# Kernel tuning notes

Measured on AMD Instinct MI355X. Metric: run time of the kernel, lower is better.

Reference implementation:

```python
import jax, jax.numpy as jnp
import numpy as np

EPS = 1e-05

def setup_inputs() -> dict:
    key = jax.random.key(0)
    k1, k2, k3 = jax.random.split(key, 3)
    B, S, D_IN, D_OUT = 4, 2048, 4096, 12288
    x = jax.random.normal(k1, (B, S, D_IN), dtype=jnp.float32)
    weight = jax.random.normal(k2, (D_OUT, D_IN), dtype=jnp.float32) * (1.0 / np.sqrt(D_IN))
    bias = jnp.zeros((D_OUT,), dtype=jnp.float32)
    ln_weight = jnp.ones((D_IN,), dtype=jnp.float32)
    ln_bias = jnp.zeros((D_IN,), dtype=jnp.float32)
    return {"x": x, "weight": weight, "bias": bias, "ln_weight": ln_weight, "ln_bias": ln_bias}

def reference(x, weight, bias, ln_weight, ln_bias):
    # LayerNorm over last dim
    mean = jnp.mean(x, axis=-1, keepdims=True)
    var = jnp.mean(jnp.square(x - mean), axis=-1, keepdims=True)
    normed = (x - mean) * jax.lax.rsqrt(var + EPS) * ln_weight + ln_bias
    # Linear: y = normed @ W^T + b
    return jnp.einsum('bsd,od->bso', normed, weight) + bias
```

## Files before the change

kernel.cpp:

```cpp
#include <hip/hip_runtime.h>
#include <hip/hip_bf16.h>
#include <stdint.h>

typedef __attribute__((ext_vector_type(8))) short short8_t;
typedef __attribute__((ext_vector_type(4))) float f32x4;

__device__ __forceinline__ unsigned short f2bf(float f) {
  union { float f; unsigned int u; } a;
  a.f = f;
  unsigned int u = a.u;
  u += 0x7fffu + ((u >> 16) & 1u);
  return (unsigned short)(u >> 16);
}

__device__ __forceinline__ void gload_lds16(const void* g, void* l) {
  __builtin_amdgcn_global_load_lds(
      (const __attribute__((address_space(1))) void*)g,
      (__attribute__((address_space(3))) void*)l, 16, 0, 0);
}

constexpr int D_IN = 4096;

__global__ __launch_bounds__(256) void ln_bf16_kernel(
    const float* __restrict__ x, const float* __restrict__ lnw,
    const float* __restrict__ lnb, unsigned short* __restrict__ out) {
  const int row = blockIdx.x;
  const int tid = threadIdx.x;
  const float* xr = x + (size_t)row * D_IN;

  f32x4 v[4];
  float sum = 0.f, sq = 0.f;
#pragma unroll
  for (int i = 0; i < 4; ++i) {
    v[i] = __builtin_nontemporal_load(
        reinterpret_cast<const f32x4*>(xr + i * 1024 + tid * 4));
    sum += v[i][0] + v[i][1] + v[i][2] + v[i][3];
    sq += v[i][0]*v[i][0] + v[i][1]*v[i][1] + v[i][2]*v[i][2] + v[i][3]*v[i][3];
  }
#pragma unroll
  for (int off = 32; off > 0; off >>= 1) {
    sum += __shfl_down(sum, off, 64);
    sq  += __shfl_down(sq, off, 64);
  }
  __shared__ float s_sum[4], s_sq[4];
  if ((tid & 63) == 0) { s_sum[tid >> 6] = sum; s_sq[tid >> 6] = sq; }
  __syncthreads();
  const float fs = s_sum[0] + s_sum[1] + s_sum[2] + s_sum[3];
  const float fq = s_sq[0] + s_sq[1] + s_sq[2] + s_sq[3];
  const float mean = fs * (1.f / D_IN);
  const float var = fq * (1.f / D_IN) - mean * mean;
  const float rstd = rsqrtf(var + 1e-5f);

  unsigned short* orow = out + (size_t)row * D_IN;
#pragma unroll
  for (int i = 0; i < 4; ++i) {
    const int col = i * 1024 + tid * 4;
    const f32x4 w = *reinterpret_cast<const f32x4*>(lnw + col);
    const f32x4 b = *reinterpret_cast<const f32x4*>(lnb + col);
    ushort4 o;
    o.x = f2bf((v[i][0] - mean) * rstd * w[0] + b[0]);
    o.y = f2bf((v[i][1] - mean) * rstd * w[1] + b[1]);
    o.z = f2bf((v[i][2] - mean) * rstd * w[2] + b[2]);
    o.w = f2bf((v[i][3] - mean) * rstd * w[3] + b[3]);
    *reinterpret_cast<ushort4*>(orow + col) = o;
  }
}

__global__ __launch_bounds__(256) void f32_to_bf16_kernel(
    const float* __restrict__ in, unsigned short* __restrict__ out) {
  const size_t i = ((size_t)blockIdx.x * 256 + threadIdx.x) * 8;
  const f32x4 a = __builtin_nontemporal_load(reinterpret_cast<const f32x4*>(in + i));
  const f32x4 b = __builtin_nontemporal_load(reinterpret_cast<const f32x4*>(in + i + 4));
  ushort4 lo, hi;
  lo.x = f2bf(a[0]); lo.y = f2bf(a[1]); lo.z = f2bf(a[2]); lo.w = f2bf(a[3]);
  hi.x = f2bf(b[0]); hi.y = f2bf(b[1]); hi.z = f2bf(b[2]); hi.w = f2bf(b[3]);
  *reinterpret_cast<ushort4*>(out + i) = lo;
  *reinterpret_cast<ushort4*>(out + i + 4) = hi;
}


#define RDA(S, KK, ROW) \
  (*reinterpret_cast<const short8_t*>(((KK) ? aB1 : aB0) + (S)*32768 + (ROW)*128))
#define RDB(S, KK, ROW) \
  (*reinterpret_cast<const short8_t*>(((KK) ? bB1 : bB0) + (S)*32768 + (ROW)*128))

#define READ_A(S, MH)                                          \
  _Pragma("unroll") for (int m_ = 0; m_ < 4; ++m_) {           \
    af[m_][0] = RDA(S, 0, (MH)*64 + m_*16);                    \
    af[m_][1] = RDA(S, 1, (MH)*64 + m_*16);                    \
  }

#define READ_B(S, NH)                                          \
  _Pragma("unroll") for (int n_ = 0; n_ < 2; ++n_) {           \
    bfr[(NH)*2+n_][0] = RDB(S, 0, ((NH)*2+n_)*16);             \
    bfr[(NH)*2+n_][1] = RDB(S, 1, ((NH)*2+n_)*16);             \
  }

#define MFMA_Q(MH, NH)                                                         \
  _Pragma("unroll") for (int kk_ = 0; kk_ < 2; ++kk_) {                        \
    _Pragma("unroll") for (int m_ = 0; m_ < 4; ++m_) {                         \
      _Pragma("unroll") for (int n_ = 0; n_ < 2; ++n_)                         \
        acc[(MH)*4+m_][(NH)*2+n_] = __builtin_amdgcn_mfma_f32_16x16x32_bf16(   \
            af[m_][kk_], bfr[(NH)*2+n_][kk_], acc[(MH)*4+m_][(NH)*2+n_], 0, 0, 0); \
    }                                                                          \
  }

#define STAGE_A(S, U, KT) \
  gload_lds16(aSrc + (size_t)((U)*64) * K + (size_t)(KT)*64, ldsAw + (S)*32768 + (U)*8192)
#define STAGE_B(S, U, KT) \
  gload_lds16(bSrc + (size_t)((U)*64) * K + (size_t)(KT)*64, ldsBw + (S)*32768 + (U)*8192)
#define STAGE_ALL(S, KT)                                       \
  STAGE_A(S,0,KT); STAGE_A(S,1,KT); STAGE_A(S,2,KT); STAGE_A(S,3,KT); \
  STAGE_B(S,0,KT); STAGE_B(S,1,KT); STAGE_B(S,2,KT); STAGE_B(S,3,KT);

#define XREG(S)                                                \
  READ_A(S, 0) READ_B(S, 0)                                    \
  __builtin_amdgcn_s_setprio(1);                               \
  MFMA_Q(0,0)                                                  \
  READ_B(S, 1)                                                 \
  MFMA_Q(0,1)                                                  \
  READ_A(S, 1)                                                 \
  __builtin_amdgcn_s_setprio(0);                               \
  asm volatile("s_waitcnt lgkmcnt(0)" ::: "memory");           \
  __builtin_amdgcn_s_barrier();                                \
  asm volatile("" ::: "memory");

#define YREG(S, KT)                                            \
  STAGE_ALL(S, KT)                                             \
  __builtin_amdgcn_s_setprio(1);                               \
  MFMA_Q(1,0)                                                  \
  MFMA_Q(1,1)                                                  \
  __builtin_amdgcn_s_setprio(0);                               \
  asm volatile("s_waitcnt vmcnt(8)" ::: "memory");             \
  __builtin_amdgcn_s_barrier();                                \
  asm volatile("" ::: "memory");

__global__ __launch_bounds__(512, 2) void gemm_xy(
    const unsigned short* __restrict__ A,
    const unsigned short* __restrict__ B,
    const float* __restrict__ bias,
    float* __restrict__ C,
    int M, int N, int K, int NYB, int BXP) {
  extern __shared__ char smem[];
  const int tid = threadIdx.x;
  const int lane = tid & 63;
  const int wid = tid >> 6;
  const int wr = wid >> 2, wc = wid & 3;
  const int fr = lane & 15;
  const int q16 = (lane >> 4) * 16;
  const int wr128 = wr * 128;
  const int wc64 = wc * 64;

  const int id = blockIdx.x;
  const int xcd = id & 7;
  const int s = id >> 3;
  const int gsz = 8 * BXP;
  const int g = s / gsz;
  const int j = s - g * gsz;
  const int by = g * 8 + (j & 7);
  const int bx = xcd * BXP + (j >> 3);
  const int m0 = by * 256, n0 = bx * 256;

  const int s_log = (tid * 16) ^ (((tid >> 3) & 7) << 4);
  const int rsw = s_log >> 7;
  const int csw = (s_log & 127) >> 1;
  const unsigned short* aSrc = A + (size_t)(m0 + rsw) * K + csw;
  const unsigned short* bSrc = B + (size_t)(n0 + rsw) * K + csw;

  char* const ldsAw = smem + wid * 1024;
  char* const ldsBw = smem + 65536 + wid * 1024;

  const int s7 = (fr & 7) << 4;
  const char* const aB0 = smem + (wr128 + fr) * 128 + (q16 ^ s7);
  const char* const aB1 = smem + (wr128 + fr) * 128 + ((64 + q16) ^ s7);
  const char* const bB0 = smem + 65536 + (wc64 + fr) * 128 + (q16 ^ s7);
  const char* const bB1 = smem + 65536 + (wc64 + fr) * 128 + ((64 + q16) ^ s7);

  f32x4 acc[8][4] = {};
  short8_t af[4][2], bfr[4][2];

  STAGE_ALL(0, 0)
  STAGE_ALL(1, 1)
  asm volatile("s_waitcnt vmcnt(8)" ::: "memory");
  __builtin_amdgcn_s_barrier();
  asm volatile("" ::: "memory");

  const int NK = K >> 6;
  for (int t = 0; t < (NK - 2) >> 1; ++t) {
    const int k2 = 2*t + 2, k3 = 2*t + 3;
    XREG(0) YREG(0, k2)
    XREG(1) YREG(1, k3)
  }
  {
    READ_A(0, 0) READ_B(0, 0)
    __builtin_amdgcn_s_setprio(1);
    MFMA_Q(0,0)
    READ_B(0, 1)
    MFMA_Q(0,1)
    READ_A(0, 1)
    MFMA_Q(1,0)
    MFMA_Q(1,1)
    __builtin_amdgcn_s_setprio(0);
    asm volatile("s_waitcnt lgkmcnt(0)\n\ts_waitcnt vmcnt(0)" ::: "memory");
    __builtin_amdgcn_s_barrier();
    asm volatile("" ::: "memory");
    READ_A(1, 0) READ_B(1, 0)
    __builtin_amdgcn_s_setprio(1);
    MFMA_Q(0,0)
    READ_B(1, 1)
    MFMA_Q(0,1)
    READ_A(1, 1)
    MFMA_Q(1,0)
    MFMA_Q(1,1)
    __builtin_amdgcn_s_setprio(0);
  }

  __syncthreads();
  float* const buf0 = (float*)smem;
  float* const buf1 = (float*)smem + 64 * 260;
  const int cr = (lane >> 4) * 4;
  float bv[4];
#pragma unroll
  for (int ni = 0; ni < 4; ++ni) bv[ni] = bias[n0 + wc64 + ni * 16 + fr];

#pragma unroll
  for (int half = 0; half < 2; ++half) {
    float* const wbuf = (wr == 0) ? buf0 : buf1;
#pragma unroll
    for (int mi4 = 0; mi4 < 4; ++mi4) {
      const int mi = half * 4 + mi4;
#pragma unroll
      for (int j2 = 0; j2 < 4; ++j2) {
        const int lr = mi4 * 16 + cr + j2;
#pragma unroll
        for (int ni = 0; ni < 4; ++ni)
          wbuf[lr * 260 + wc64 + ni * 16 + fr] = acc[mi][ni][j2] + bv[ni];
      }
    }
    __syncthreads();
#pragma unroll
    for (int i = 0; i < 16; ++i) {
      const int idx = wid * 16 + i;
      const float* src = (idx < 64 ? buf0 + idx * 260 : buf1 + (idx - 64) * 260) + lane * 4;
      const int grow = m0 + (idx < 64 ? half * 64 + idx : 128 + half * 64 + (idx - 64));
      const f32x4 vv = *reinterpret_cast<const f32x4*>(src);
      __builtin_nontemporal_store(
          vv, reinterpret_cast<f32x4*>(C + (size_t)grow * N + n0) + lane);
    }
    __syncthreads();
  }
}

extern "C" void kernel_launch(void* const* d_in, const int* in_sizes, int n_in,
                              void* d_out, int out_size, void* d_ws, size_t ws_size,
                              hipStream_t stream) {
  const float* x    = (const float*)d_in[0];
  const float* w    = (const float*)d_in[1];
  const float* bias = (const float*)d_in[2];
  const float* lnw  = (const float*)d_in[3];
  const float* lnb  = (const float*)d_in[4];
  float* out = (float*)d_out;

  const int DIN  = 4096;
  const int M    = in_sizes[0] / DIN;
  const int DOUT = in_sizes[2];

  unsigned short* normA = (unsigned short*)d_ws;
  unsigned short* wB    = normA + (size_t)M * DIN;

  ln_bf16_kernel<<<M, 256, 0, stream>>>(x, lnw, lnb, normA);
  f32_to_bf16_kernel<<<((size_t)DOUT * DIN) / (256 * 8), 256, 0, stream>>>(w, wB);

  const int nwg = (M / 256) * (DOUT / 256);
  const int smem_bytes = 2 * 64 * 260 * 4 > 131072 ? 2 * 64 * 260 * 4 : 131072;
  (void)hipFuncSetAttribute((const void*)gemm_xy,
                            hipFuncAttributeMaxDynamicSharedMemorySize, 163840);
  gemm_xy<<<nwg, 512, smem_bytes, stream>>>(normA, wB, bias, out,
                                            M, DOUT, DIN, M / 256, (DOUT / 256) / 8);
}
```

Baseline: 729.9 us.

## Split GEMM tile across 16 waves of 64x64 instead of 8 waves

```diff
diff --git a/kernel.cpp b/kernel.cpp
--- a/kernel.cpp
+++ b/kernel.cpp
@@ -84,13 +84,13 @@
 #define RDB(S, KK, ROW) \
   (*reinterpret_cast<const short8_t*>(((KK) ? bB1 : bB0) + (S)*32768 + (ROW)*128))
 
-#define READ_A(S, MH)                                          \
-  _Pragma("unroll") for (int m_ = 0; m_ < 4; ++m_) {           \
-    af[m_][0] = RDA(S, 0, (MH)*64 + m_*16);                    \
-    af[m_][1] = RDA(S, 1, (MH)*64 + m_*16);                    \
-  }
-
-#define READ_B(S, NH)                                          \
+#define READ_A2(S, MH)                                         \
+  _Pragma("unroll") for (int m_ = 0; m_ < 2; ++m_) {           \
+    af[(MH)*2+m_][0] = RDA(S, 0, ((MH)*2+m_)*16);              \
+    af[(MH)*2+m_][1] = RDA(S, 1, ((MH)*2+m_)*16);              \
+  }
+
+#define READ_B2(S, NH)                                         \
   _Pragma("unroll") for (int n_ = 0; n_ < 2; ++n_) {           \
     bfr[(NH)*2+n_][0] = RDB(S, 0, ((NH)*2+n_)*16);             \
     bfr[(NH)*2+n_][1] = RDB(S, 1, ((NH)*2+n_)*16);             \
@@ -98,28 +98,27 @@
 
 #define MFMA_Q(MH, NH)                                                         \
   _Pragma("unroll") for (int kk_ = 0; kk_ < 2; ++kk_) {                        \
-    _Pragma("unroll") for (int m_ = 0; m_ < 4; ++m_) {                         \
+    _Pragma("unroll") for (int m_ = 0; m_ < 2; ++m_) {                         \
       _Pragma("unroll") for (int n_ = 0; n_ < 2; ++n_)                         \
-        acc[(MH)*4+m_][(NH)*2+n_] = __builtin_amdgcn_mfma_f32_16x16x32_bf16(   \
-            af[m_][kk_], bfr[(NH)*2+n_][kk_], acc[(MH)*4+m_][(NH)*2+n_], 0, 0, 0); \
+        acc[(MH)*2+m_][(NH)*2+n_] = __builtin_amdgcn_mfma_f32_16x16x32_bf16(   \
+            af[(MH)*2+m_][kk_], bfr[(NH)*2+n_][kk_], acc[(MH)*2+m_][(NH)*2+n_], 0, 0, 0); \
     }                                                                          \
   }
 
 #define STAGE_A(S, U, KT) \
-  gload_lds16(aSrc + (size_t)((U)*64) * K + (size_t)(KT)*64, ldsAw + (S)*32768 + (U)*8192)
+  gload_lds16(aSrc + (size_t)((U)*128) * K + (size_t)(KT)*64, ldsAw + (S)*32768 + (U)*16384)
 #define STAGE_B(S, U, KT) \
-  gload_lds16(bSrc + (size_t)((U)*64) * K + (size_t)(KT)*64, ldsBw + (S)*32768 + (U)*8192)
+  gload_lds16(bSrc + (size_t)((U)*128) * K + (size_t)(KT)*64, ldsBw + (S)*32768 + (U)*16384)
 #define STAGE_ALL(S, KT)                                       \
-  STAGE_A(S,0,KT); STAGE_A(S,1,KT); STAGE_A(S,2,KT); STAGE_A(S,3,KT); \
-  STAGE_B(S,0,KT); STAGE_B(S,1,KT); STAGE_B(S,2,KT); STAGE_B(S,3,KT);
+  STAGE_A(S,0,KT); STAGE_A(S,1,KT); STAGE_B(S,0,KT); STAGE_B(S,1,KT);
 
 #define XREG(S)                                                \
-  READ_A(S, 0) READ_B(S, 0)                                    \
+  READ_A2(S, 0) READ_B2(S, 0)                                  \
   __builtin_amdgcn_s_setprio(1);                               \
   MFMA_Q(0,0)                                                  \
-  READ_B(S, 1)                                                 \
+  READ_B2(S, 1)                                                \
   MFMA_Q(0,1)                                                  \
-  READ_A(S, 1)                                                 \
+  READ_A2(S, 1)                                                \
   __builtin_amdgcn_s_setprio(0);                               \
   asm volatile("s_waitcnt lgkmcnt(0)" ::: "memory");           \
   __builtin_amdgcn_s_barrier();                                \
@@ -131,11 +130,11 @@
   MFMA_Q(1,0)                                                  \
   MFMA_Q(1,1)                                                  \
   __builtin_amdgcn_s_setprio(0);                               \
-  asm volatile("s_waitcnt vmcnt(8)" ::: "memory");             \
+  asm volatile("s_waitcnt vmcnt(4)" ::: "memory");             \
   __builtin_amdgcn_s_barrier();                                \
   asm volatile("" ::: "memory");
 
-__global__ __launch_bounds__(512, 2) void gemm_xy(
+__global__ __launch_bounds__(1024, 4) void gemm_xy16(
     const unsigned short* __restrict__ A,
     const unsigned short* __restrict__ B,
     const float* __restrict__ bias,
@@ -148,8 +147,6 @@
   const int wr = wid >> 2, wc = wid & 3;
   const int fr = lane & 15;
   const int q16 = (lane >> 4) * 16;
-  const int wr128 = wr * 128;
-  const int wc64 = wc * 64;
 
   const int id = blockIdx.x;
   const int xcd = id & 7;
@@ -171,17 +168,17 @@
   char* const ldsBw = smem + 65536 + wid * 1024;
 
   const int s7 = (fr & 7) << 4;
-  const char* const aB0 = smem + (wr128 + fr) * 128 + (q16 ^ s7);
-  const char* const aB1 = smem + (wr128 + fr) * 128 + ((64 + q16) ^ s7);
-  const char* const bB0 = smem + 65536 + (wc64 + fr) * 128 + (q16 ^ s7);
-  const char* const bB1 = smem + 65536 + (wc64 + fr) * 128 + ((64 + q16) ^ s7);
-
-  f32x4 acc[8][4] = {};
+  const char* const aB0 = smem + (wr * 64 + fr) * 128 + (q16 ^ s7);
+  const char* const aB1 = smem + (wr * 64 + fr) * 128 + ((64 + q16) ^ s7);
+  const char* const bB0 = smem + 65536 + (wc * 64 + fr) * 128 + (q16 ^ s7);
+  const char* const bB1 = smem + 65536 + (wc * 64 + fr) * 128 + ((64 + q16) ^ s7);
+
+  f32x4 acc[4][4] = {};
   short8_t af[4][2], bfr[4][2];
 
   STAGE_ALL(0, 0)
   STAGE_ALL(1, 1)
-  asm volatile("s_waitcnt vmcnt(8)" ::: "memory");
+  asm volatile("s_waitcnt vmcnt(4)" ::: "memory");
   __builtin_amdgcn_s_barrier();
   asm volatile("" ::: "memory");
 
@@ -192,58 +189,56 @@
     XREG(1) YREG(1, k3)
   }
   {
-    READ_A(0, 0) READ_B(0, 0)
+    READ_A2(0, 0) READ_B2(0, 0)
     __builtin_amdgcn_s_setprio(1);
     MFMA_Q(0,0)
-    READ_B(0, 1)
+    READ_B2(0, 1)
     MFMA_Q(0,1)
-    READ_A(0, 1)
+    READ_A2(0, 1)
     MFMA_Q(1,0)
     MFMA_Q(1,1)
     __builtin_amdgcn_s_setprio(0);
     asm volatile("s_waitcnt lgkmcnt(0)\n\ts_waitcnt vmcnt(0)" ::: "memory");
     __builtin_amdgcn_s_barrier();
     asm volatile("" ::: "memory");
-    READ_A(1, 0) READ_B(1, 0)
+    READ_A2(1, 0) READ_B2(1, 0)
     __builtin_amdgcn_s_setprio(1);
     MFMA_Q(0,0)
-    READ_B(1, 1)
+    READ_B2(1, 1)
     MFMA_Q(0,1)
-    READ_A(1, 1)
+    READ_A2(1, 1)
     MFMA_Q(1,0)
     MFMA_Q(1,1)
     __builtin_amdgcn_s_setprio(0);
   }
 
   __syncthreads();
-  float* const buf0 = (float*)smem;
-  float* const buf1 = (float*)smem + 64 * 260;
+  float* const buf = (float*)smem;
   const int cr = (lane >> 4) * 4;
   float bv[4];
 #pragma unroll
-  for (int ni = 0; ni < 4; ++ni) bv[ni] = bias[n0 + wc64 + ni * 16 + fr];
-
-#pragma unroll
-  for (int half = 0; half < 2; ++half) {
-    float* const wbuf = (wr == 0) ? buf0 : buf1;
-#pragma unroll
-    for (int mi4 = 0; mi4 < 4; ++mi4) {
-      const int mi = half * 4 + mi4;
-#pragma unroll
-      for (int j2 = 0; j2 < 4; ++j2) {
-        const int lr = mi4 * 16 + cr + j2;
-#pragma unroll
-        for (int ni = 0; ni < 4; ++ni)
-          wbuf[lr * 260 + wc64 + ni * 16 + fr] = acc[mi][ni][j2] + bv[ni];
+  for (int ni = 0; ni < 4; ++ni) bv[ni] = bias[n0 + wc * 64 + ni * 16 + fr];
+
+#pragma unroll
+  for (int half = 0; half < 4; ++half) {
+    if (wr == half) {
+#pragma unroll
+      for (int mi = 0; mi < 4; ++mi) {
+#pragma unroll
+        for (int jj = 0; jj < 4; ++jj) {
+          const int lr = mi * 16 + cr + jj;
+#pragma unroll
+          for (int ni = 0; ni < 4; ++ni)
+            buf[lr * 260 + wc * 64 + ni * 16 + fr] = acc[mi][ni][jj] + bv[ni];
+        }
       }
     }
     __syncthreads();
 #pragma unroll
-    for (int i = 0; i < 16; ++i) {
-      const int idx = wid * 16 + i;
-      const float* src = (idx < 64 ? buf0 + idx * 260 : buf1 + (idx - 64) * 260) + lane * 4;
-      const int grow = m0 + (idx < 64 ? half * 64 + idx : 128 + half * 64 + (idx - 64));
-      const f32x4 vv = *reinterpret_cast<const f32x4*>(src);
+    for (int i = 0; i < 4; ++i) {
+      const int idx = wid * 4 + i;
+      const f32x4 vv = *reinterpret_cast<const f32x4*>(buf + idx * 260 + lane * 4);
+      const int grow = m0 + half * 64 + idx;
       __builtin_nontemporal_store(
           vv, reinterpret_cast<f32x4*>(C + (size_t)grow * N + n0) + lane);
     }
@@ -272,9 +267,8 @@
   f32_to_bf16_kernel<<<((size_t)DOUT * DIN) / (256 * 8), 256, 0, stream>>>(w, wB);
 
   const int nwg = (M / 256) * (DOUT / 256);
-  const int smem_bytes = 2 * 64 * 260 * 4 > 131072 ? 2 * 64 * 260 * 4 : 131072;
-  (void)hipFuncSetAttribute((const void*)gemm_xy,
-                            hipFuncAttributeMaxDynamicSharedMemorySize, 163840);
-  gemm_xy<<<nwg, 512, smem_bytes, stream>>>(normA, wB, bias, out,
-                                            M, DOUT, DIN, M / 256, (DOUT / 256) / 8);
-}
+  (void)hipFuncSetAttribute((const void*)gemm_xy16,
+                            hipFuncAttributeMaxDynamicSharedMemorySize, 131072);
+  gemm_xy16<<<nwg, 1024, 131072, stream>>>(normA, wB, bias, out,
+                                           M, DOUT, DIN, M / 256, (DOUT / 256) / 8);
+}
```

New measurement: 1.486 ms. 104% more time.
